# Performance work log

Hardware: AMD Instinct MI355X
Metric: run time of the kernel (lower is better)

## Reference

```python
import jax, jax.numpy as jnp
import numpy as np

EMBED_DIM = 256
NUM_HEADS = 8
QKV_DIM = EMBED_DIM  # qkv_dim_ratio = 1
HEAD_DIM = QKV_DIM // NUM_HEADS  # 32


def setup_inputs() -> dict:
    key = jax.random.key(0)
    ks = jax.random.split(key, 6)
    B, C, H, W = 1, EMBED_DIM, 64, 64
    s = 0.02
    return {
        "x": jax.random.normal(ks[0], (B, C, H, W), dtype=jnp.float32),
        "wq": jax.random.normal(ks[1], (QKV_DIM, C), dtype=jnp.float32) * s,
        "wk": jax.random.normal(ks[2], (QKV_DIM, C), dtype=jnp.float32) * s,
        "wv": jax.random.normal(ks[3], (QKV_DIM, C), dtype=jnp.float32) * s,
        "wo": jax.random.normal(ks[4], (C, QKV_DIM), dtype=jnp.float32) * s,
        "wl": jax.random.normal(ks[5], (C, 1, 3, 3), dtype=jnp.float32) * s,
    }


def _mhsa(x, wq, wk, wv, wo, wl):
    B, C, H, W = x.shape
    N = H * W
    xf = x.reshape(B, C, N)  # 1x1 conv == channel matmul
    def proj(w):
        # [B, qkv, N] -> [B, heads, N, head_dim]
        y = jnp.einsum('oc,bcn->bon', w, xf)
        return y.reshape(B, NUM_HEADS, HEAD_DIM, N).transpose(0, 1, 3, 2)
    q, k, v = proj(wq), proj(wk), proj(wv)
    scale = HEAD_DIM ** -0.5
    attn = jax.nn.softmax(jnp.einsum('bhnd,bhmd->bhnm', q, k) * scale, axis=-1)
    out = jnp.einsum('bhnm,bhmd->bhnd', attn, v)  # [B, h, N, d]
    out = out.transpose(0, 1, 3, 2).reshape(B, QKV_DIM, N)
    attn_out = jnp.einsum('co,bon->bcn', wo, out).reshape(B, C, H, W)
    local_out = jax.lax.conv_general_dilated(
        x, wl, window_strides=(1, 1), padding=((1, 1), (1, 1)),
        dimension_numbers=('NCHW', 'OIHW', 'NCHW'), feature_group_count=C)
    return local_out + attn_out


def reference(x, wq, wk, wv, wo, wl):
    return _mhsa(x, wq, wk, wv, wo, wl)
```

## Files before the change

kernel.cpp:

```cpp
#include <hip/hip_runtime.h>

#define N_TOK 4096
#define C_DIM 256
#define HEADS 8
#define HDIM  32
#define KSPLIT 2
#define QSCALE 0.17677669529663687f
#define L2E    1.4426950408889634f

typedef __attribute__((ext_vector_type(8))) short bf16x8;
typedef __attribute__((ext_vector_type(4))) float f32x4;
typedef __attribute__((ext_vector_type(4))) unsigned int u32x4;
typedef __attribute__((ext_vector_type(8))) unsigned short u16x8;

static __device__ __forceinline__ unsigned short f2bf(float f) {
  union { float f; unsigned int u; } c; c.f = f;
  return (unsigned short)((c.u + 0x8000u) >> 16);
}
static __device__ __forceinline__ float bf2f(unsigned short u) {
  union { unsigned int i; float f; } c; c.i = ((unsigned int)u) << 16;
  return c.f;
}
static __device__ __forceinline__ float fexp2(float x) {
  float r; asm("v_exp_f32 %0, %1" : "=v"(r) : "v"(x)); return r;
}
static __device__ __forceinline__ unsigned int cvt_pk(float lo, float hi) {
  unsigned int r; asm("v_cvt_pk_bf16_f32 %0, %1, %2" : "=v"(r) : "v"(lo), "v"(hi)); return r;
}

__global__ __launch_bounds__(256) void wsplit(
    const float* __restrict__ wq, const float* __restrict__ wk,
    const float* __restrict__ wv, const float* __restrict__ wo,
    unsigned short* __restrict__ Whi, unsigned short* __restrict__ Wlo)
{
  const int i4  = blockIdx.x * 256 + threadIdx.x;
  const int idx = i4 * 4;
  const int r   = idx >> 8;
  const float* src; int off; float scl = 1.f;
  if (r < 256)      { src = wq; off = idx;          scl = QSCALE * L2E; }
  else if (r < 512) { src = wk; off = idx - 65536;  }
  else if (r < 768) { src = wv; off = idx - 131072; }
  else              { src = wo; off = idx - 196608; }
  float4 v = *reinterpret_cast<const float4*>(&src[off]);
  v.x *= scl; v.y *= scl; v.z *= scl; v.w *= scl;
  ushort4 h, l;
  h.x = f2bf(v.x); l.x = f2bf(v.x - bf2f(h.x));
  h.y = f2bf(v.y); l.y = f2bf(v.y - bf2f(h.y));
  h.z = f2bf(v.z); l.z = f2bf(v.z - bf2f(h.z));
  h.w = f2bf(v.w); l.w = f2bf(v.w - bf2f(h.w));
  *reinterpret_cast<ushort4*>(&Whi[idx]) = h;
  *reinterpret_cast<ushort4*>(&Wlo[idx]) = l;
}

__global__ __launch_bounds__(256) void tsplit(
    const float* __restrict__ src,
    unsigned short* __restrict__ dhi, unsigned short* __restrict__ dlo)
{
  __shared__ float T[64][69];
  const int c0 = blockIdx.y * 64, n0 = blockIdx.x * 64;
  const int t = threadIdx.x;
  {
    const int cl = t >> 2, ng = (t & 3) * 16;
    #pragma unroll
    for (int jj = 0; jj < 4; jj++) {
      const float4 v = *reinterpret_cast<const float4*>(&src[(c0 + cl) * N_TOK + n0 + ng + jj * 4]);
      T[cl][ng + jj * 4 + 0] = v.x; T[cl][ng + jj * 4 + 1] = v.y;
      T[cl][ng + jj * 4 + 2] = v.z; T[cl][ng + jj * 4 + 3] = v.w;
    }
  }
  __syncthreads();
  {
    const int nl = t >> 2, cg = (t & 3) * 16;
    u16x8 h0, h1, l0, l1;
    #pragma unroll
    for (int j = 0; j < 8; j++) {
      const float v = T[cg + j][nl];
      h0[j] = f2bf(v); l0[j] = f2bf(v - bf2f(h0[j]));
    }
    #pragma unroll
    for (int j = 0; j < 8; j++) {
      const float v = T[cg + 8 + j][nl];
      h1[j] = f2bf(v); l1[j] = f2bf(v - bf2f(h1[j]));
    }
    const size_t base = (size_t)(n0 + nl) * C_DIM + c0 + cg;
    *reinterpret_cast<u16x8*>(&dhi[base])     = h0;
    *reinterpret_cast<u16x8*>(&dhi[base + 8]) = h1;
    *reinterpret_cast<u16x8*>(&dlo[base])     = l0;
    *reinterpret_cast<u16x8*>(&dlo[base + 8]) = l1;
  }
}

__global__ __launch_bounds__(256) void qkv_mfma(
    const unsigned short* __restrict__ Whi, const unsigned short* __restrict__ Wlo,
    const unsigned short* __restrict__ Xhi, const unsigned short* __restrict__ Xlo,
    unsigned short* __restrict__ Qkv, unsigned short* __restrict__ Kt)
{
  const int n0 = blockIdx.x * 64;
  const int by = blockIdx.y;
  const int tid = threadIdx.x;
  const int w = tid >> 6, lane = tid & 63, lq = lane & 15, g = lane >> 4;
  const int o0 = by * 64 + w * 16;

  __shared__ unsigned short Bs[2][4096];

  const int e0l = tid & 63, e0f = tid >> 6;
  const unsigned short* s0p; const unsigned short* s1p;
  {
    const int lq_ = e0l & 15, g_ = e0l >> 4;
    const int f0 = e0f, f1 = e0f + 4;
    s0p = ((f0 & 1) ? Xlo : Xhi) + (size_t)(n0 + (f0 >> 1) * 16 + lq_) * C_DIM + 8 * g_;
    s1p = ((f1 & 1) ? Xlo : Xhi) + (size_t)(n0 + (f1 >> 1) * 16 + lq_) * C_DIM + 8 * g_;
  }
  const unsigned short* ahp = &Whi[(size_t)(o0 + lq) * C_DIM + 8 * g];
  const unsigned short* alp = &Wlo[(size_t)(o0 + lq) * C_DIM + 8 * g];

  f32x4 acc[4] = {{0.f,0.f,0.f,0.f},{0.f,0.f,0.f,0.f},{0.f,0.f,0.f,0.f},{0.f,0.f,0.f,0.f}};

  bf16x8 ah = *reinterpret_cast<const bf16x8*>(ahp);
  bf16x8 al = *reinterpret_cast<const bf16x8*>(alp);
  {
    const bf16x8 b0 = *reinterpret_cast<const bf16x8*>(s0p);
    const bf16x8 b1 = *reinterpret_cast<const bf16x8*>(s1p);
    *reinterpret_cast<bf16x8*>(&Bs[0][(size_t)tid * 8]) = b0;
    *reinterpret_cast<bf16x8*>(&Bs[0][((size_t)tid + 256) * 8]) = b1;
  }
  __syncthreads();

  int cur = 0;
  #pragma unroll
  for (int kk = 0; kk < 8; kk++) {
    bf16x8 nb0 = {}, nb1 = {}, nah = {}, nal = {};
    if (kk < 7) {
      const int ko = (kk + 1) * 32;
      nb0 = *reinterpret_cast<const bf16x8*>(s0p + ko);
      nb1 = *reinterpret_cast<const bf16x8*>(s1p + ko);
      nah = *reinterpret_cast<const bf16x8*>(ahp + ko);
      nal = *reinterpret_cast<const bf16x8*>(alp + ko);
    }
    #pragma unroll
    for (int ns = 0; ns < 4; ns++) {
      const bf16x8 bh = *reinterpret_cast<const bf16x8*>(&Bs[cur][(size_t)((ns * 2 + 0) * 64 + lane) * 8]);
      const bf16x8 bl = *reinterpret_cast<const bf16x8*>(&Bs[cur][(size_t)((ns * 2 + 1) * 64 + lane) * 8]);
      acc[ns] = __builtin_amdgcn_mfma_f32_16x16x32_bf16(ah, bh, acc[ns], 0, 0, 0);
      acc[ns] = __builtin_amdgcn_mfma_f32_16x16x32_bf16(ah, bl, acc[ns], 0, 0, 0);
      acc[ns] = __builtin_amdgcn_mfma_f32_16x16x32_bf16(al, bh, acc[ns], 0, 0, 0);
    }
    if (kk < 7) {
      *reinterpret_cast<bf16x8*>(&Bs[cur ^ 1][(size_t)tid * 8]) = nb0;
      *reinterpret_cast<bf16x8*>(&Bs[cur ^ 1][((size_t)tid + 256) * 8]) = nb1;
      ah = nah; al = nal;
    }
    __syncthreads();
    cur ^= 1;
  }

  if (by < 4 || by >= 8) {
    const int orow0 = (by < 4 ? by * 64 : (by - 8) * 64 + 512) + w * 16 + 4 * g;
    #pragma unroll
    for (int ns = 0; ns < 4; ns++)
      #pragma unroll
      for (int r = 0; r < 4; r++)
        Qkv[(size_t)(orow0 + r) * N_TOK + n0 + ns * 16 + lq] = f2bf(acc[ns][r]);
  } else {
    const int ok0 = (by - 4) * 64 + w * 16 + 4 * g;
    const int hh = ok0 >> 5, d0 = ok0 & 31;
    #pragma unroll
    for (int ns = 0; ns < 4; ns++) {
      ushort4 u;
      u.x = f2bf(acc[ns][0]); u.y = f2bf(acc[ns][1]);
      u.z = f2bf(acc[ns][2]); u.w = f2bf(acc[ns][3]);
      *reinterpret_cast<ushort4*>(&Kt[((size_t)hh * N_TOK + n0 + ns * 16 + lq) * HDIM + d0]) = u;
    }
  }
}

__global__ __launch_bounds__(256) void dwconv_kernel(
    const float* __restrict__ x, const float* __restrict__ wl,
    float* __restrict__ out)
{
  const int idx = blockIdx.x * 256 + threadIdx.x;
  const int c  = idx >> 12;
  const int yy = (idx >> 6) & 63;
  const int xx = idx & 63;
  const float* xc = x + c * 4096;
  const float* wc = wl + c * 9;
  float acc = 0.f;
  #pragma unroll
  for (int dy = 0; dy < 3; dy++) {
    const int y = yy + dy - 1;
    if (y < 0 || y > 63) continue;
    #pragma unroll
    for (int dx = 0; dx < 3; dx++) {
      const int x2 = xx + dx - 1;
      if (x2 < 0 || x2 > 63) continue;
      acc += wc[dy * 3 + dx] * xc[y * 64 + x2];
    }
  }
  out[idx] = acc;
}

__global__ __launch_bounds__(256) void attn_mfma(
    const unsigned short* __restrict__ Qkv,
    const unsigned short* __restrict__ Kt,
    float* __restrict__ Opart,
    float* __restrict__ lpart)
{
  const int h  = blockIdx.z;
  const int ks = blockIdx.y;
  const int tid  = threadIdx.x;
  const int w    = tid >> 6;
  const int lane = tid & 63;
  const int lq   = lane & 15;
  const int g    = lane >> 4;
  const int nq   = blockIdx.x * 64 + w * 16 + lq;

  __shared__ unsigned short KbL[2][2048];
  __shared__ unsigned short VbL[2][2048];

  bf16x8 qf;
  {
    const unsigned short* Qh = Qkv + h * HDIM * N_TOK;
    #pragma unroll
    for (int j = 0; j < 8; j++) qf[j] = (short)Qh[(8 * g + j) * N_TOK + nq];
  }

  const unsigned short* KtH = Kt + (size_t)h * N_TOK * HDIM;
  const unsigned short* VH  = Qkv + (512 + h * HDIM) * N_TOK;
  const int kbase = ks * (N_TOK / KSPLIT);
  const int pr = 8 * (lq >> 2) + (lq & 3);

  const int skey  = (w & 1) * 4 + (w >> 1) * 32 + pr;
  const unsigned short* ksrc = &KtH[(size_t)(kbase + skey) * HDIM + 8 * g];
  const int sdrow = (w & 1) * 16 + lq;
  const unsigned short* vsrc = &VH[(size_t)sdrow * N_TOK + kbase + (w >> 1) * 32 + 8 * g];

  {
    const bf16x8 kr = *reinterpret_cast<const bf16x8*>(ksrc);
    const bf16x8 vr = *reinterpret_cast<const bf16x8*>(vsrc);
    *reinterpret_cast<bf16x8*>(&KbL[0][tid * 8]) = kr;
    *reinterpret_cast<bf16x8*>(&VbL[0][tid * 8]) = vr;
  }
  __syncthreads();

  f32x4 o0 = {0.f,0.f,0.f,0.f}, o1 = {0.f,0.f,0.f,0.f};
  f32x4 la0 = {0.f,0.f,0.f,0.f}, la1 = {0.f,0.f,0.f,0.f};
  const f32x4 zz = {0.f,0.f,0.f,0.f};
  constexpr int NT = (N_TOK / KSPLIT) / 64;

  int cur = 0;
  #pragma unroll 2
  for (int t = 0; t < NT; ++t) {
    bf16x8 kr = {}, vr = {};
    if (t + 1 < NT) {
      kr = *reinterpret_cast<const bf16x8*>(ksrc + (size_t)(t + 1) * 64 * HDIM);
      vr = *reinterpret_cast<const bf16x8*>(vsrc + (t + 1) * 64);
    }

    const unsigned short* kb = &KbL[cur][0];
    const unsigned short* vb = &VbL[cur][0];
    const bf16x8 kf0 = *reinterpret_cast<const bf16x8*>(&kb[lane * 8]);
    const bf16x8 kf1 = *reinterpret_cast<const bf16x8*>(&kb[lane * 8 + 512]);
    const bf16x8 kf2 = *reinterpret_cast<const bf16x8*>(&kb[lane * 8 + 1024]);
    const bf16x8 kf3 = *reinterpret_cast<const bf16x8*>(&kb[lane * 8 + 1536]);

    const f32x4 s0 = __builtin_amdgcn_mfma_f32_16x16x32_bf16(kf0, qf, zz, 0, 0, 0);
    const f32x4 s1 = __builtin_amdgcn_mfma_f32_16x16x32_bf16(kf1, qf, zz, 0, 0, 0);
    const f32x4 s2 = __builtin_amdgcn_mfma_f32_16x16x32_bf16(kf2, qf, zz, 0, 0, 0);
    const f32x4 s3 = __builtin_amdgcn_mfma_f32_16x16x32_bf16(kf3, qf, zz, 0, 0, 0);

    f32x4 p0, p1, p2, p3;
    #pragma unroll
    for (int r = 0; r < 4; r++) {
      p0[r] = fexp2(s0[r]); p1[r] = fexp2(s1[r]);
      p2[r] = fexp2(s2[r]); p3[r] = fexp2(s3[r]);
    }
    la0 += p0; la0 += p1; la1 += p2; la1 += p3;

    const u32x4 pua = { cvt_pk(p0[0], p0[1]), cvt_pk(p0[2], p0[3]),
                        cvt_pk(p1[0], p1[1]), cvt_pk(p1[2], p1[3]) };
    const u32x4 pub = { cvt_pk(p2[0], p2[1]), cvt_pk(p2[2], p2[3]),
                        cvt_pk(p3[0], p3[1]), cvt_pk(p3[2], p3[3]) };
    const bf16x8 pfa = __builtin_bit_cast(bf16x8, pua);
    const bf16x8 pfb = __builtin_bit_cast(bf16x8, pub);

    const bf16x8 vf0a = *reinterpret_cast<const bf16x8*>(&vb[lane * 8]);
    const bf16x8 vf1a = *reinterpret_cast<const bf16x8*>(&vb[lane * 8 + 512]);
    const bf16x8 vf0b = *reinterpret_cast<const bf16x8*>(&vb[lane * 8 + 1024]);
    const bf16x8 vf1b = *reinterpret_cast<const bf16x8*>(&vb[lane * 8 + 1536]);

    o0 = __builtin_amdgcn_mfma_f32_16x16x32_bf16(vf0a, pfa, o0, 0, 0, 0);
    o0 = __builtin_amdgcn_mfma_f32_16x16x32_bf16(vf0b, pfb, o0, 0, 0, 0);
    o1 = __builtin_amdgcn_mfma_f32_16x16x32_bf16(vf1a, pfa, o1, 0, 0, 0);
    o1 = __builtin_amdgcn_mfma_f32_16x16x32_bf16(vf1b, pfb, o1, 0, 0, 0);

    if (t + 1 < NT) {
      *reinterpret_cast<bf16x8*>(&KbL[cur ^ 1][tid * 8]) = kr;
      *reinterpret_cast<bf16x8*>(&VbL[cur ^ 1][tid * 8]) = vr;
    }
    __syncthreads();
    cur ^= 1;
  }

  float ls = (la0[0] + la0[1]) + (la0[2] + la0[3]) + (la1[0] + la1[1]) + (la1[2] + la1[3]);
  ls += __shfl_xor(ls, 16);
  ls += __shfl_xor(ls, 32);

  const int ob = (ks * HEADS + h) * HDIM;
  #pragma unroll
  for (int r = 0; r < 4; r++) {
    Opart[(size_t)(ob + 4 * g + r) * N_TOK + nq]      = o0[r];
    Opart[(size_t)(ob + 16 + 4 * g + r) * N_TOK + nq] = o1[r];
  }
  if (g == 0) lpart[(ks * HEADS + h) * N_TOK + nq] = ls;
}

__global__ __launch_bounds__(256) void combsplit(
    const float* __restrict__ Opart, const float* __restrict__ lpart,
    unsigned short* __restrict__ dhi, unsigned short* __restrict__ dlo)
{
  __shared__ float T[64][69];
  __shared__ float Linv[2][64];
  const int o0 = blockIdx.y * 64, n0 = blockIdx.x * 64;
  const int t = threadIdx.x;
  if (t < 128) {
    const int hl = t >> 6, nl = t & 63;
    const int hh = (o0 >> 5) + hl;
    float L = 0.f;
    #pragma unroll
    for (int ks = 0; ks < KSPLIT; ks++)
      L += lpart[(ks * HEADS + hh) * N_TOK + n0 + nl];
    Linv[hl][nl] = 1.f / L;
  }
  __syncthreads();
  {
    const int cl = t >> 2, ng = (t & 3) * 16;
    const int hrow = cl >> 5;
    #pragma unroll
    for (int jj = 0; jj < 4; jj++) {
      float4 a = make_float4(0.f, 0.f, 0.f, 0.f);
      #pragma unroll
      for (int ks = 0; ks < KSPLIT; ks++) {
        const float4 v = *reinterpret_cast<const float4*>(
            &Opart[(size_t)ks * C_DIM * N_TOK + (size_t)(o0 + cl) * N_TOK + n0 + ng + jj * 4]);
        a.x += v.x; a.y += v.y; a.z += v.z; a.w += v.w;
      }
      T[cl][ng + jj * 4 + 0] = a.x * Linv[hrow][ng + jj * 4 + 0];
      T[cl][ng + jj * 4 + 1] = a.y * Linv[hrow][ng + jj * 4 + 1];
      T[cl][ng + jj * 4 + 2] = a.z * Linv[hrow][ng + jj * 4 + 2];
      T[cl][ng + jj * 4 + 3] = a.w * Linv[hrow][ng + jj * 4 + 3];
    }
  }
  __syncthreads();
  {
    const int nl = t >> 2, cg = (t & 3) * 16;
    u16x8 h0, h1, l0, l1;
    #pragma unroll
    for (int j = 0; j < 8; j++) {
      const float v = T[cg + j][nl];
      h0[j] = f2bf(v); l0[j] = f2bf(v - bf2f(h0[j]));
    }
    #pragma unroll
    for (int j = 0; j < 8; j++) {
      const float v = T[cg + 8 + j][nl];
      h1[j] = f2bf(v); l1[j] = f2bf(v - bf2f(h1[j]));
    }
    const size_t base = (size_t)(n0 + nl) * C_DIM + o0 + cg;
    *reinterpret_cast<u16x8*>(&dhi[base])     = h0;
    *reinterpret_cast<u16x8*>(&dhi[base + 8]) = h1;
    *reinterpret_cast<u16x8*>(&dlo[base])     = l0;
    *reinterpret_cast<u16x8*>(&dlo[base + 8]) = l1;
  }
}

__global__ __launch_bounds__(256) void out_mfma(
    const unsigned short* __restrict__ Whi, const unsigned short* __restrict__ Wlo,
    const unsigned short* __restrict__ Ohi, const unsigned short* __restrict__ Olo,
    float* __restrict__ out)
{
  const int n0 = blockIdx.x * 64;
  const int by = blockIdx.y;
  const int kb = blockIdx.z * 128;
  const int tid = threadIdx.x;
  const int w = tid >> 6, lane = tid & 63, lq = lane & 15, g = lane >> 4;
  const int c0 = by * 64 + w * 16;

  __shared__ unsigned short Bs[2][4096];

  const int e0l = tid & 63, e0f = tid >> 6;
  const unsigned short* s0p; const unsigned short* s1p;
  {
    const int lq_ = e0l & 15, g_ = e0l >> 4;
    const int f0 = e0f, f1 = e0f + 4;
    s0p = ((f0 & 1) ? Olo : Ohi) + (size_t)(n0 + (f0 >> 1) * 16 + lq_) * C_DIM + kb + 8 * g_;
    s1p = ((f1 & 1) ? Olo : Ohi) + (size_t)(n0 + (f1 >> 1) * 16 + lq_) * C_DIM + kb + 8 * g_;
  }
  const unsigned short* ahp = &Whi[(size_t)(768 + c0 + lq) * C_DIM + kb + 8 * g];
  const unsigned short* alp = &Wlo[(size_t)(768 + c0 + lq) * C_DIM + kb + 8 * g];

  f32x4 acc[4] = {{0.f,0.f,0.f,0.f},{0.f,0.f,0.f,0.f},{0.f,0.f,0.f,0.f},{0.f,0.f,0.f,0.f}};

  bf16x8 ah = *reinterpret_cast<const bf16x8*>(ahp);
  bf16x8 al = *reinterpret_cast<const bf16x8*>(alp);
  {
    const bf16x8 b0 = *reinterpret_cast<const bf16x8*>(s0p);
    const bf16x8 b1 = *reinterpret_cast<const bf16x8*>(s1p);
    *reinterpret_cast<bf16x8*>(&Bs[0][(size_t)tid * 8]) = b0;
    *reinterpret_cast<bf16x8*>(&Bs[0][((size_t)tid + 256) * 8]) = b1;
  }
  __syncthreads();

  int cur = 0;
  #pragma unroll
  for (int kk = 0; kk < 4; kk++) {
    bf16x8 nb0 = {}, nb1 = {}, nah = {}, nal = {};
    if (kk < 3) {
      const int ko = (kk + 1) * 32;
      nb0 = *reinterpret_cast<const bf16x8*>(s0p + ko);
      nb1 = *reinterpret_cast<const bf16x8*>(s1p + ko);
      nah = *reinterpret_cast<const bf16x8*>(ahp + ko);
      nal = *reinterpret_cast<const bf16x8*>(alp + ko);
    }
    #pragma unroll
    for (int ns = 0; ns < 4; ns++) {
      const bf16x8 bh = *reinterpret_cast<const bf16x8*>(&Bs[cur][(size_t)((ns * 2 + 0) * 64 + lane) * 8]);
      const bf16x8 bl = *reinterpret_cast<const bf16x8*>(&Bs[cur][(size_t)((ns * 2 + 1) * 64 + lane) * 8]);
      acc[ns] = __builtin_amdgcn_mfma_f32_16x16x32_bf16(ah, bh, acc[ns], 0, 0, 0);
      acc[ns] = __builtin_amdgcn_mfma_f32_16x16x32_bf16(ah, bl, acc[ns], 0, 0, 0);
      acc[ns] = __builtin_amdgcn_mfma_f32_16x16x32_bf16(al, bh, acc[ns], 0, 0, 0);
    }
    if (kk < 3) {
      *reinterpret_cast<bf16x8*>(&Bs[cur ^ 1][(size_t)tid * 8]) = nb0;
      *reinterpret_cast<bf16x8*>(&Bs[cur ^ 1][((size_t)tid + 256) * 8]) = nb1;
      ah = nah; al = nal;
    }
    __syncthreads();
    cur ^= 1;
  }

  #pragma unroll
  for (int ns = 0; ns < 4; ns++)
    #pragma unroll
    for (int r = 0; r < 4; r++)
      unsafeAtomicAdd(&out[(size_t)(c0 + 4 * g + r) * N_TOK + n0 + ns * 16 + lq], acc[ns][r]);
}

extern "C" void kernel_launch(void* const* d_in, const int* in_sizes, int n_in,
                              void* d_out, int out_size, void* d_ws, size_t ws_size,
                              hipStream_t stream) {
  const float* x  = (const float*)d_in[0];
  const float* wq = (const float*)d_in[1];
  const float* wk = (const float*)d_in[2];
  const float* wv = (const float*)d_in[3];
  const float* wo = (const float*)d_in[4];
  const float* wl = (const float*)d_in[5];
  float* out = (float*)d_out;

  float* Opart = (float*)d_ws;
  float* lpart = Opart + (size_t)KSPLIT * C_DIM * N_TOK;
  unsigned short* Qkv = (unsigned short*)(lpart + KSPLIT * HEADS * N_TOK);
  unsigned short* Kt  = Qkv + 768 * N_TOK;
  unsigned short* Whi = Kt + (size_t)HEADS * N_TOK * HDIM;
  unsigned short* Wlo = Whi + 1024 * C_DIM;
  unsigned short* Xhi = Wlo + 1024 * C_DIM;
  unsigned short* Xlo = Xhi + (size_t)N_TOK * C_DIM;
  unsigned short* Ohi = Xlo + (size_t)N_TOK * C_DIM;
  unsigned short* Olo = Ohi + (size_t)N_TOK * C_DIM;

  wsplit<<<256, 256, 0, stream>>>(wq, wk, wv, wo, Whi, Wlo);
  tsplit<<<dim3(64, 4), 256, 0, stream>>>(x, Xhi, Xlo);
  qkv_mfma<<<dim3(64, 12), 256, 0, stream>>>(Whi, Wlo, Xhi, Xlo, Qkv, Kt);
  dwconv_kernel<<<4096, 256, 0, stream>>>(x, wl, out);
  attn_mfma<<<dim3(64, KSPLIT, HEADS), 256, 0, stream>>>(Qkv, Kt, Opart, lpart);
  combsplit<<<dim3(64, 4), 256, 0, stream>>>(Opart, lpart, Ohi, Olo);
  out_mfma<<<dim3(64, 4, 2), 256, 0, stream>>>(Whi, Wlo, Ohi, Olo, out);
}
```

Measured before the change: 136.3 us.

## Process two query tiles per wave in attention and raise key split to four

Each wave now computes two 16-query tiles against the same K/V shared-memory tiles, so every K/V load from LDS and global memory feeds twice as much MFMA work. To keep the grid size unchanged, the query grid is halved and the key dimension is split four ways instead of two. This trades more registers per thread and larger partial-output buffers and combine work for less K/V traffic per query.

```diff
diff --git a/kernel.cpp b/kernel.cpp
--- a/kernel.cpp
+++ b/kernel.cpp
@@ -4,7 +4,7 @@
 #define C_DIM 256
 #define HEADS 8
 #define HDIM  32
-#define KSPLIT 2
+#define KSPLIT 4
 #define QSCALE 0.17677669529663687f
 #define L2E    1.4426950408889634f
 
@@ -212,16 +212,20 @@
   const int lane = tid & 63;
   const int lq   = lane & 15;
   const int g    = lane >> 4;
-  const int nq   = blockIdx.x * 64 + w * 16 + lq;
+  const int nqa  = blockIdx.x * 128 + w * 32 + lq;
+  const int nqb  = nqa + 16;
 
   __shared__ unsigned short KbL[2][2048];
   __shared__ unsigned short VbL[2][2048];
 
-  bf16x8 qf;
+  bf16x8 qfa, qfb;
   {
     const unsigned short* Qh = Qkv + h * HDIM * N_TOK;
     #pragma unroll
-    for (int j = 0; j < 8; j++) qf[j] = (short)Qh[(8 * g + j) * N_TOK + nq];
+    for (int j = 0; j < 8; j++) {
+      qfa[j] = (short)Qh[(8 * g + j) * N_TOK + nqa];
+      qfb[j] = (short)Qh[(8 * g + j) * N_TOK + nqb];
+    }
   }
 
   const unsigned short* KtH = Kt + (size_t)h * N_TOK * HDIM;
@@ -242,8 +246,9 @@
   }
   __syncthreads();
 
-  f32x4 o0 = {0.f,0.f,0.f,0.f}, o1 = {0.f,0.f,0.f,0.f};
-  f32x4 la0 = {0.f,0.f,0.f,0.f}, la1 = {0.f,0.f,0.f,0.f};
+  f32x4 o0a = {0.f,0.f,0.f,0.f}, o1a = {0.f,0.f,0.f,0.f};
+  f32x4 o0b = {0.f,0.f,0.f,0.f}, o1b = {0.f,0.f,0.f,0.f};
+  f32x4 laa = {0.f,0.f,0.f,0.f}, lab = {0.f,0.f,0.f,0.f};
   const f32x4 zz = {0.f,0.f,0.f,0.f};
   constexpr int NT = (N_TOK / KSPLIT) / 64;
 
@@ -263,35 +268,53 @@
     const bf16x8 kf2 = *reinterpret_cast<const bf16x8*>(&kb[lane * 8 + 1024]);
     const bf16x8 kf3 = *reinterpret_cast<const bf16x8*>(&kb[lane * 8 + 1536]);
 
-    const f32x4 s0 = __builtin_amdgcn_mfma_f32_16x16x32_bf16(kf0, qf, zz, 0, 0, 0);
-    const f32x4 s1 = __builtin_amdgcn_mfma_f32_16x16x32_bf16(kf1, qf, zz, 0, 0, 0);
-    const f32x4 s2 = __builtin_amdgcn_mfma_f32_16x16x32_bf16(kf2, qf, zz, 0, 0, 0);
-    const f32x4 s3 = __builtin_amdgcn_mfma_f32_16x16x32_bf16(kf3, qf, zz, 0, 0, 0);
-
-    f32x4 p0, p1, p2, p3;
+    f32x4 s0 = __builtin_amdgcn_mfma_f32_16x16x32_bf16(kf0, qfa, zz, 0, 0, 0);
+    f32x4 s1 = __builtin_amdgcn_mfma_f32_16x16x32_bf16(kf1, qfa, zz, 0, 0, 0);
+    f32x4 s2 = __builtin_amdgcn_mfma_f32_16x16x32_bf16(kf2, qfa, zz, 0, 0, 0);
+    f32x4 s3 = __builtin_amdgcn_mfma_f32_16x16x32_bf16(kf3, qfa, zz, 0, 0, 0);
     #pragma unroll
     for (int r = 0; r < 4; r++) {
-      p0[r] = fexp2(s0[r]); p1[r] = fexp2(s1[r]);
-      p2[r] = fexp2(s2[r]); p3[r] = fexp2(s3[r]);
-    }
-    la0 += p0; la0 += p1; la1 += p2; la1 += p3;
-
-    const u32x4 pua = { cvt_pk(p0[0], p0[1]), cvt_pk(p0[2], p0[3]),
-                        cvt_pk(p1[0], p1[1]), cvt_pk(p1[2], p1[3]) };
-    const u32x4 pub = { cvt_pk(p2[0], p2[1]), cvt_pk(p2[2], p2[3]),
-                        cvt_pk(p3[0], p3[1]), cvt_pk(p3[2], p3[3]) };
-    const bf16x8 pfa = __builtin_bit_cast(bf16x8, pua);
-    const bf16x8 pfb = __builtin_bit_cast(bf16x8, pub);
+      s0[r] = fexp2(s0[r]); s1[r] = fexp2(s1[r]);
+      s2[r] = fexp2(s2[r]); s3[r] = fexp2(s3[r]);
+    }
+    laa += s0; laa += s1; laa += s2; laa += s3;
+    const u32x4 pua_a = { cvt_pk(s0[0], s0[1]), cvt_pk(s0[2], s0[3]),
+                          cvt_pk(s1[0], s1[1]), cvt_pk(s1[2], s1[3]) };
+    const u32x4 pub_a = { cvt_pk(s2[0], s2[1]), cvt_pk(s2[2], s2[3]),
+                          cvt_pk(s3[0], s3[1]), cvt_pk(s3[2], s3[3]) };
+    const bf16x8 pfa_a = __builtin_bit_cast(bf16x8, pua_a);
+    const bf16x8 pfb_a = __builtin_bit_cast(bf16x8, pub_a);
+
+    f32x4 t0 = __builtin_amdgcn_mfma_f32_16x16x32_bf16(kf0, qfb, zz, 0, 0, 0);
+    f32x4 t1 = __builtin_amdgcn_mfma_f32_16x16x32_bf16(kf1, qfb, zz, 0, 0, 0);
+    f32x4 t2 = __builtin_amdgcn_mfma_f32_16x16x32_bf16(kf2, qfb, zz, 0, 0, 0);
+    f32x4 t3 = __builtin_amdgcn_mfma_f32_16x16x32_bf16(kf3, qfb, zz, 0, 0, 0);
+    #pragma unroll
+    for (int r = 0; r < 4; r++) {
+      t0[r] = fexp2(t0[r]); t1[r] = fexp2(t1[r]);
+      t2[r] = fexp2(t2[r]); t3[r] = fexp2(t3[r]);
+    }
+    lab += t0; lab += t1; lab += t2; lab += t3;
+    const u32x4 pua_b = { cvt_pk(t0[0], t0[1]), cvt_pk(t0[2], t0[3]),
+                          cvt_pk(t1[0], t1[1]), cvt_pk(t1[2], t1[3]) };
+    const u32x4 pub_b = { cvt_pk(t2[0], t2[1]), cvt_pk(t2[2], t2[3]),
+                          cvt_pk(t3[0], t3[1]), cvt_pk(t3[2], t3[3]) };
+    const bf16x8 pfa_b = __builtin_bit_cast(bf16x8, pua_b);
+    const bf16x8 pfb_b = __builtin_bit_cast(bf16x8, pub_b);
 
     const bf16x8 vf0a = *reinterpret_cast<const bf16x8*>(&vb[lane * 8]);
     const bf16x8 vf1a = *reinterpret_cast<const bf16x8*>(&vb[lane * 8 + 512]);
     const bf16x8 vf0b = *reinterpret_cast<const bf16x8*>(&vb[lane * 8 + 1024]);
     const bf16x8 vf1b = *reinterpret_cast<const bf16x8*>(&vb[lane * 8 + 1536]);
 
-    o0 = __builtin_amdgcn_mfma_f32_16x16x32_bf16(vf0a, pfa, o0, 0, 0, 0);
-    o0 = __builtin_amdgcn_mfma_f32_16x16x32_bf16(vf0b, pfb, o0, 0, 0, 0);
-    o1 = __builtin_amdgcn_mfma_f32_16x16x32_bf16(vf1a, pfa, o1, 0, 0, 0);
-    o1 = __builtin_amdgcn_mfma_f32_16x16x32_bf16(vf1b, pfb, o1, 0, 0, 0);
+    o0a = __builtin_amdgcn_mfma_f32_16x16x32_bf16(vf0a, pfa_a, o0a, 0, 0, 0);
+    o0a = __builtin_amdgcn_mfma_f32_16x16x32_bf16(vf0b, pfb_a, o0a, 0, 0, 0);
+    o1a = __builtin_amdgcn_mfma_f32_16x16x32_bf16(vf1a, pfa_a, o1a, 0, 0, 0);
+    o1a = __builtin_amdgcn_mfma_f32_16x16x32_bf16(vf1b, pfb_a, o1a, 0, 0, 0);
+    o0b = __builtin_amdgcn_mfma_f32_16x16x32_bf16(vf0a, pfa_b, o0b, 0, 0, 0);
+    o0b = __builtin_amdgcn_mfma_f32_16x16x32_bf16(vf0b, pfb_b, o0b, 0, 0, 0);
+    o1b = __builtin_amdgcn_mfma_f32_16x16x32_bf16(vf1a, pfa_b, o1b, 0, 0, 0);
+    o1b = __builtin_amdgcn_mfma_f32_16x16x32_bf16(vf1b, pfb_b, o1b, 0, 0, 0);
 
     if (t + 1 < NT) {
       *reinterpret_cast<bf16x8*>(&KbL[cur ^ 1][tid * 8]) = kr;
@@ -301,17 +324,25 @@
     cur ^= 1;
   }
 
-  float ls = (la0[0] + la0[1]) + (la0[2] + la0[3]) + (la1[0] + la1[1]) + (la1[2] + la1[3]);
-  ls += __shfl_xor(ls, 16);
-  ls += __shfl_xor(ls, 32);
+  float lsa = (laa[0] + laa[1]) + (laa[2] + laa[3]);
+  lsa += __shfl_xor(lsa, 16);
+  lsa += __shfl_xor(lsa, 32);
+  float lsb = (lab[0] + lab[1]) + (lab[2] + lab[3]);
+  lsb += __shfl_xor(lsb, 16);
+  lsb += __shfl_xor(lsb, 32);
 
   const int ob = (ks * HEADS + h) * HDIM;
   #pragma unroll
   for (int r = 0; r < 4; r++) {
-    Opart[(size_t)(ob + 4 * g + r) * N_TOK + nq]      = o0[r];
-    Opart[(size_t)(ob + 16 + 4 * g + r) * N_TOK + nq] = o1[r];
-  }
-  if (g == 0) lpart[(ks * HEADS + h) * N_TOK + nq] = ls;
+    Opart[(size_t)(ob + 4 * g + r) * N_TOK + nqa]      = o0a[r];
+    Opart[(size_t)(ob + 16 + 4 * g + r) * N_TOK + nqa] = o1a[r];
+    Opart[(size_t)(ob + 4 * g + r) * N_TOK + nqb]      = o0b[r];
+    Opart[(size_t)(ob + 16 + 4 * g + r) * N_TOK + nqb] = o1b[r];
+  }
+  if (g == 0) {
+    lpart[(ks * HEADS + h) * N_TOK + nqa] = lsa;
+    lpart[(ks * HEADS + h) * N_TOK + nqb] = lsb;
+  }
 }
 
 __global__ __launch_bounds__(256) void combsplit(
@@ -470,7 +501,7 @@
   tsplit<<<dim3(64, 4), 256, 0, stream>>>(x, Xhi, Xlo);
   qkv_mfma<<<dim3(64, 12), 256, 0, stream>>>(Whi, Wlo, Xhi, Xlo, Qkv, Kt);
   dwconv_kernel<<<4096, 256, 0, stream>>>(x, wl, out);
-  attn_mfma<<<dim3(64, KSPLIT, HEADS), 256, 0, stream>>>(Qkv, Kt, Opart, lpart);
+  attn_mfma<<<dim3(32, KSPLIT, HEADS), 256, 0, stream>>>(Qkv, Kt, Opart, lpart);
   combsplit<<<dim3(64, 4), 256, 0, stream>>>(Opart, lpart, Ohi, Olo);
   out_mfma<<<dim3(64, 4, 2), 256, 0, stream>>>(Whi, Wlo, Ohi, Olo, out);
 }
```

Result: slower. 142.5 us (+4.5%).
